# Kernel tuning notes

Measured on AMD Instinct MI355X. Metric: run time of the kernel, lower is better.

## Reference

```python
import jax, jax.numpy as jnp
from jax import lax
import numpy as np
import math

B, W, C, H, K = 4, 1024, 1024, 16, 3  # batch, frames(cropsize), bins, num_bands, kernel
D = C // H  # head dim


def setup_inputs() -> dict:
    key = jax.random.key(0)
    ks = jax.random.split(key, 17)
    lin = lambda k: jax.random.normal(k, (C, C), jnp.float32) * 0.02
    vec = lambda k: jax.random.normal(k, (C,), jnp.float32) * 0.02
    cw = lambda k: jax.random.normal(k, (C, 1, K), jnp.float32) * 0.2  # depthwise conv weight (O, I/g=1, K)
    return {
        'x': jax.random.normal(ks[0], (B, W, C), jnp.float32),
        'qW': lin(ks[1]), 'qb': vec(ks[2]), 'qcw': cw(ks[3]), 'qcb': vec(ks[4]),
        'kW': lin(ks[5]), 'kb': vec(ks[6]), 'kcw': cw(ks[7]), 'kcb': vec(ks[8]),
        'vW': lin(ks[9]), 'vb': vec(ks[10]), 'vcw': cw(ks[11]), 'vcb': vec(ks[12]),
        'oW': lin(ks[13]), 'ob': vec(ks[14]),
        'er': jax.random.normal(ks[15], (D, W), jnp.float32),
    }


def _causal_dwconv(x_bwc, w, b):
    # x: (B, W, C) -> conv over time with left pad K-1, depthwise (groups=C)
    y = lax.conv_general_dilated(
        x_bwc.transpose(0, 2, 1), w, window_strides=(1,), padding=[(K - 1, 0)],
        feature_group_count=C, dimension_numbers=('NCH', 'OIH', 'NCH'))
    return (y + b[None, :, None]).transpose(0, 2, 1)


def reference(x, qW, qb, qcw, qcb, kW, kb, kcw, kcb, vW, vb, vcw, vcb, oW, ob, er):
    q = _causal_dwconv(x @ qW.T + qb, qcw, qcb).reshape(B, W, H, D).transpose(0, 2, 1, 3)  # bhwd
    k = _causal_dwconv(x @ kW.T + kb, kcw, kcb).reshape(B, W, H, D).transpose(0, 2, 3, 1)  # bhdw
    v = _causal_dwconv(x @ vW.T + vb, vcw, vcb).reshape(B, W, H, D).transpose(0, 2, 1, 3)  # bhwd
    # Music-Transformer relative position skewing
    p = jnp.pad(jnp.einsum('bhwd,dt->bhwt', q, er), ((0, 0), (0, 0), (0, 0), (1, 0)))
    p = p.transpose(0, 1, 3, 2)[:, :, 1:, :]  # (B,H,W,W)
    qk = (jnp.matmul(q, k) + p) / math.sqrt(C)
    a = jax.nn.softmax(qk, axis=-1)
    o = jnp.matmul(a, v).transpose(0, 2, 1, 3).reshape(B, W, C)
    return o @ oW.T + ob
```

## Files before the change

### kernel.cpp

```cpp
#include <hip/hip_runtime.h>

#define B_ 4
#define W_ 1024
#define C_ 1024
#define H_ 16
#define D_ 64

typedef __attribute__((ext_vector_type(8))) short short8;
typedef __attribute__((ext_vector_type(4))) float f32x4;

__device__ __forceinline__ unsigned short f2b(float f) {
  unsigned u = __builtin_bit_cast(unsigned, f);
  unsigned r = (u + 0x7fffu + ((u >> 16) & 1u)) >> 16;
  return (unsigned short)r;
}
__device__ __forceinline__ float b2f(short b) {
  return __builtin_bit_cast(float, ((unsigned)(unsigned short)b) << 16);
}
__device__ __forceinline__ unsigned pk2(float a, float b) {
  unsigned r;
  asm("v_cvt_pk_bf16_f32 %0, %1, %2" : "=v"(r) : "v"(a), "v"(b));
  return r;
}

typedef __attribute__((address_space(1))) void GV;
typedef __attribute__((address_space(3))) void LV;
__device__ __forceinline__ void gl16(const short* g, short* l) {
  __builtin_amdgcn_global_load_lds((GV*)g, (LV*)l, 16, 0, 0);
}

__global__ __launch_bounds__(256)
void prep_kernel(const float* __restrict__ x, const float* __restrict__ qW,
                 const float* __restrict__ kW, const float* __restrict__ vW,
                 const float* __restrict__ oW, const float* __restrict__ er,
                 short* __restrict__ xh, short* __restrict__ wh,
                 short* __restrict__ ertb) {
  const int bx = blockIdx.x;
  const int tid = threadIdx.x;
  if (bx < 4096) {
    const float* s;
    short* d;
    size_t u;
    if (bx < 2048) {
      u = (size_t)bx * 256 + tid;
      s = x; d = xh;
    } else {
      u = (size_t)(bx - 2048) * 256 + tid;
      const int w = (int)(u >> 17);
      s = (w == 0) ? qW : (w == 1) ? kW : (w == 2) ? vW : oW;
      d = wh + (u & ~(size_t)131071) * 8;
      u &= 131071;
      const float4* p = (const float4*)s + u * 2;
      float4 a = p[0], b = p[1];
      short8 r;
      r[0] = f2b(a.x); r[1] = f2b(a.y); r[2] = f2b(a.z); r[3] = f2b(a.w);
      r[4] = f2b(b.x); r[5] = f2b(b.y); r[6] = f2b(b.z); r[7] = f2b(b.w);
      *((short8*)d + u) = r;
      return;
    }
    const float4* p = (const float4*)s + u * 2;
    float4 a = p[0], b = p[1];
    short8 r;
    r[0] = f2b(a.x); r[1] = f2b(a.y); r[2] = f2b(a.z); r[3] = f2b(a.w);
    r[4] = f2b(b.x); r[5] = f2b(b.y); r[6] = f2b(b.z); r[7] = f2b(b.w);
    *((short8*)d + u) = r;
  } else {
    int i = (bx - 4096) * 256 + tid;
    int d = i >> 8;
    int w4 = (i & 255) << 2;
    float4 v = *(const float4*)(er + (size_t)d * W_ + w4);
    ertb[(size_t)(w4 + 0) * D_ + d] = f2b(v.x);
    ertb[(size_t)(w4 + 1) * D_ + d] = f2b(v.y);
    ertb[(size_t)(w4 + 2) * D_ + d] = f2b(v.z);
    ertb[(size_t)(w4 + 3) * D_ + d] = f2b(v.w);
  }
}

#define GSTAGE(T, BUF)                                                       \
  {                                                                          \
    const int k0_ = (T) * 64;                                                \
    gl16(ga + (size_t)0  * K + k0_, sA[BUF] + 0    + ldst);                  \
    gl16(gb + (size_t)0  * K + k0_, sB[BUF] + 0    + ldst);                  \
    gl16(ga + (size_t)32 * K + k0_, sA[BUF] + 2048 + ldst);                  \
    gl16(gb + (size_t)32 * K + k0_, sB[BUF] + 2048 + ldst);                  \
    gl16(ga + (size_t)64 * K + k0_, sA[BUF] + 4096 + ldst);                  \
    gl16(gb + (size_t)64 * K + k0_, sB[BUF] + 4096 + ldst);                  \
    gl16(ga + (size_t)96 * K + k0_, sA[BUF] + 6144 + ldst);                  \
    gl16(gb + (size_t)96 * K + k0_, sB[BUF] + 6144 + ldst);                  \
  }

template <int OUTF32>
__global__ __launch_bounds__(256)
void gemm_bf16_v3(const short* __restrict__ A, const short* __restrict__ Wt,
                  const float* __restrict__ b0, const float* __restrict__ b1,
                  const float* __restrict__ b2, void* __restrict__ outv,
                  int M, int N, int K) {
  __shared__ short sA[2][128 * 64];
  __shared__ short sB[2][128 * 64];
  const int tid = threadIdx.x;
  const int bm = blockIdx.y * 128, bn = blockIdx.x * 128;
  const int wv = tid >> 6, lane = tid & 63;
  const int wr = (wv >> 1) * 64, wc = (wv & 1) * 64;
  const int l15 = lane & 15, l4 = lane >> 4;
  const int srow = tid >> 3;
  const int swsc = ((tid & 7) ^ (srow & 7)) * 8;
  const int cxor = (l15 & 7) * 8;
  const int ldst = tid * 8;
  const short* ga = A + (size_t)(bm + srow) * K + swsc;
  const short* gb = Wt + (size_t)(bn + srow) * K + swsc;

  f32x4 acc[4][4];
#pragma unroll
  for (int mf = 0; mf < 4; ++mf)
#pragma unroll
    for (int nf = 0; nf < 4; ++nf) acc[mf][nf] = (f32x4){0.f, 0.f, 0.f, 0.f};

  const int nt = K >> 6;
  GSTAGE(0, 0)
  for (int t = 0; t < nt; ++t) {
    const int cur = t & 1;
    if (t + 1 < nt) {
      GSTAGE(t + 1, cur ^ 1)
      asm volatile("s_waitcnt vmcnt(8)" ::: "memory");
    } else {
      asm volatile("s_waitcnt vmcnt(0)" ::: "memory");
    }
    __builtin_amdgcn_s_barrier();
    __builtin_amdgcn_sched_barrier(0);
#pragma unroll
    for (int ks = 0; ks < 2; ++ks) {
      short8 af[4], bf[4];
#pragma unroll
      for (int mf = 0; mf < 4; ++mf)
        af[mf] = *(short8*)(sA[cur] + (wr + mf * 16 + l15) * 64 + ((ks * 32 + l4 * 8) ^ cxor));
#pragma unroll
      for (int nf = 0; nf < 4; ++nf)
        bf[nf] = *(short8*)(sB[cur] + (wc + nf * 16 + l15) * 64 + ((ks * 32 + l4 * 8) ^ cxor));
#pragma unroll
      for (int mf = 0; mf < 4; ++mf)
#pragma unroll
        for (int nf = 0; nf < 4; ++nf)
          acc[mf][nf] = __builtin_amdgcn_mfma_f32_16x16x32_bf16(af[mf], bf[nf], acc[mf][nf], 0, 0, 0);
    }
    __builtin_amdgcn_sched_barrier(0);
    __builtin_amdgcn_s_barrier();
  }
#pragma unroll
  for (int mf = 0; mf < 4; ++mf) {
#pragma unroll
    for (int nf = 0; nf < 4; ++nf) {
      const int n = bn + wc + nf * 16 + l15;
      const float bs = (n < 1024) ? b0[n] : ((n < 2048) ? b1[n - 1024] : b2[n - 2048]);
#pragma unroll
      for (int r = 0; r < 4; ++r) {
        const int m = bm + wr + mf * 16 + l4 * 4 + r;
        const float v = acc[mf][nf][r] + bs;
        if (OUTF32) ((float*)outv)[(size_t)m * N + n] = v;
        else        ((short*)outv)[(size_t)m * N + n] = (short)f2b(v);
      }
    }
  }
}

__global__ __launch_bounds__(256)
void dwconv_qk_kernel(const short* __restrict__ yqkv,
                      const float* __restrict__ qcw, const float* __restrict__ qcb,
                      const float* __restrict__ kcw, const float* __restrict__ kcb,
                      short* __restrict__ qc, short* __restrict__ kc) {
  const int t = blockIdx.y;
  const float* cw = t ? kcw : qcw;
  const float* cb = t ? kcb : qcb;
  short* out = t ? kc : qc;
  const int idx = blockIdx.x * 256 + threadIdx.x;
  const int c8 = (idx & (C_ / 8 - 1)) << 3;
  const int bw = idx >> 7;
  const int w = bw & (W_ - 1);
  const short* base = yqkv + (size_t)bw * (3 * C_) + t * C_ + c8;
  short8 x2 = *(const short8*)base;
  short8 x1, x0;
  if (w >= 1) x1 = *(const short8*)(base - 3 * C_); else { for (int j = 0; j < 8; ++j) x1[j] = 0; }
  if (w >= 2) x0 = *(const short8*)(base - 6 * C_); else { for (int j = 0; j < 8; ++j) x0[j] = 0; }
  short8 r;
#pragma unroll
  for (int j = 0; j < 8; ++j) {
    const int c = c8 + j;
    float acc = b2f(x0[j]) * cw[c * 3 + 0] + b2f(x1[j]) * cw[c * 3 + 1] +
                b2f(x2[j]) * cw[c * 3 + 2] + cb[c];
    r[j] = (short)f2b(acc);
  }
  *(short8*)(out + (size_t)bw * C_ + c8) = r;
}

__global__ __launch_bounds__(256)
void dwconv_vt_kernel(const short* __restrict__ yqkv, const float* __restrict__ vcw,
                      const float* __restrict__ vcb, short* __restrict__ vt) {
  __shared__ short t[64][72];
  const int bh = blockIdx.y, w0 = blockIdx.x * 64;
  const int b = bh >> 4, h = bh & 15;
  const int tid = threadIdx.x;
  for (int c = tid; c < 512; c += 256) {
    const int w = c >> 3, dg = c & 7;
    const int gw = w0 + w;
    const short* base = yqkv + ((size_t)(b * W_ + gw)) * (3 * C_) + 2 * C_ + h * 64 + dg * 8;
    short8 x2 = *(const short8*)base;
    short8 x1, x0;
    if (gw >= 1) x1 = *(const short8*)(base - 3 * C_); else { for (int j = 0; j < 8; ++j) x1[j] = 0; }
    if (gw >= 2) x0 = *(const short8*)(base - 6 * C_); else { for (int j = 0; j < 8; ++j) x0[j] = 0; }
#pragma unroll
    for (int j = 0; j < 8; ++j) {
      const int ch = h * 64 + dg * 8 + j;
      float acc = b2f(x0[j]) * vcw[ch * 3 + 0] + b2f(x1[j]) * vcw[ch * 3 + 1] +
                  b2f(x2[j]) * vcw[ch * 3 + 2] + vcb[ch];
      t[dg * 8 + j][w] = (short)f2b(acc);
    }
  }
  __syncthreads();
  for (int c = tid; c < 512; c += 256) {
    const int d = c >> 3, wg = c & 7;
    *(short8*)(vt + ((size_t)(bh * 64 + d)) * W_ + w0 + wg * 8) = *(short8*)&t[d][wg * 8];
  }
}

__global__ __launch_bounds__(256)
void attn_v3_kernel(const short* __restrict__ q, const short* __restrict__ k,
                    const short* __restrict__ vt, const short* __restrict__ ert,
                    short* __restrict__ o) {
  __shared__ short sK[2][4096];
  __shared__ short sQj[2][4096];
  __shared__ short sVt[2][4096];
  __shared__ short sU[8192];
  short* sQ = sU;
  short* sE = sU + 4096;
  short* sP = sU;

  const int tid = threadIdx.x;
  const int wid = blockIdx.x;
  const int swz = (wid & 7) * 128 + (wid >> 3);
  const int bh = swz >> 4, qt = swz & 15;
  const int b = bh >> 4, h = bh & 15;
  const int i0 = qt * 64;
  const int wv = tid >> 6, lane = tid & 63;
  const int l15 = lane & 15, l4 = lane >> 4;
  const size_t bW = (size_t)b * W_;
  const int srow = tid >> 3;
  const int swsc = ((tid & 7) ^ (srow & 7)) * 8;
  const int cxor = (l15 & 7) * 8;

  const short* qbase = q + bW * C_ + h * 64;
  const short* kbase = k + bW * C_ + h * 64;
  const short* vbase = vt + (size_t)bh * 64 * W_;

  {
    const short* g;
    g = qbase + (size_t)(i0 + srow) * C_ + swsc;
    gl16(g, sQ + tid * 8); gl16(g + (size_t)32 * C_, sQ + 2048 + tid * 8);
    g = ert + (size_t)(i0 + srow) * 64 + swsc;
    gl16(g, sE + tid * 8); gl16(g + 32 * 64, sE + 2048 + tid * 8);
    g = kbase + (size_t)srow * C_ + swsc;
    gl16(g, sK[0] + tid * 8); gl16(g + (size_t)32 * C_, sK[0] + 2048 + tid * 8);
    g = qbase + (size_t)srow * C_ + swsc;
    gl16(g, sQj[0] + tid * 8); gl16(g + (size_t)32 * C_, sQj[0] + 2048 + tid * 8);
    g = vbase + (size_t)srow * W_ + swsc;
    gl16(g, sVt[0] + tid * 8); gl16(g + (size_t)32 * W_, sVt[0] + 2048 + tid * 8);
  }
  __syncthreads();

  short8 bQ[2], bE[2];
#pragma unroll
  for (int ks = 0; ks < 2; ++ks) {
    const int off = (ks * 32 + l4 * 8) ^ cxor;
    bQ[ks] = *(short8*)(sQ + (wv * 16 + l15) * 64 + off);
    bE[ks] = *(short8*)(sE + (wv * 16 + l15) * 64 + off);
  }
  __syncthreads();

  float m_ = -1e30f, l_ = 0.f;
  f32x4 accO[4];
#pragma unroll
  for (int mf = 0; mf < 4; ++mf) accO[mf] = (f32x4){0.f, 0.f, 0.f, 0.f};
  const float SC = 0.03125f;

  for (int jt = 0; jt < 16; ++jt) {
    const int cur = jt & 1;
    if (jt < 15) {
      const int j0n = (jt + 1) * 64;
      const short* g;
      g = kbase + (size_t)(j0n + srow) * C_ + swsc;
      gl16(g, sK[cur ^ 1] + tid * 8); gl16(g + (size_t)32 * C_, sK[cur ^ 1] + 2048 + tid * 8);
      g = qbase + (size_t)(j0n + srow) * C_ + swsc;
      gl16(g, sQj[cur ^ 1] + tid * 8); gl16(g + (size_t)32 * C_, sQj[cur ^ 1] + 2048 + tid * 8);
      g = vbase + (size_t)srow * W_ + j0n + swsc;
      gl16(g, sVt[cur ^ 1] + tid * 8); gl16(g + (size_t)32 * W_, sVt[cur ^ 1] + 2048 + tid * 8);
    }

    f32x4 s[4];
#pragma unroll
    for (int mf = 0; mf < 4; ++mf) s[mf] = (f32x4){0.f, 0.f, 0.f, 0.f};
    const int ofA = (l4 * 8) ^ cxor;
    const int ofB = (32 + l4 * 8) ^ cxor;
    __builtin_amdgcn_s_setprio(1);
#pragma unroll
    for (int mf = 0; mf < 4; ++mf) {
      const short* kp = sK[cur] + (mf * 16 + l15) * 64;
      const short* jp = sQj[cur] + (mf * 16 + l15) * 64;
      s[mf] = __builtin_amdgcn_mfma_f32_16x16x32_bf16(*(short8*)(kp + ofA), bQ[0], s[mf], 0, 0, 0);
      s[mf] = __builtin_amdgcn_mfma_f32_16x16x32_bf16(*(short8*)(kp + ofB), bQ[1], s[mf], 0, 0, 0);
      s[mf] = __builtin_amdgcn_mfma_f32_16x16x32_bf16(*(short8*)(jp + ofA), bE[0], s[mf], 0, 0, 0);
      s[mf] = __builtin_amdgcn_mfma_f32_16x16x32_bf16(*(short8*)(jp + ofB), bE[1], s[mf], 0, 0, 0);
    }
    __builtin_amdgcn_s_setprio(0);

    float px = fmaxf(fmaxf(s[0][0], s[0][1]), fmaxf(s[0][2], s[0][3]));
#pragma unroll
    for (int mf = 1; mf < 4; ++mf)
      px = fmaxf(px, fmaxf(fmaxf(s[mf][0], s[mf][1]), fmaxf(s[mf][2], s[mf][3])));
    px = fmaxf(px, __shfl_xor(px, 16));
    px = fmaxf(px, __shfl_xor(px, 32));
    px *= SC;
    if (!__all(px <= m_ + 8.f)) {
      const float mn = fmaxf(m_, px);
      const float sc = __expf(m_ - mn);
      l_ *= sc;
#pragma unroll
      for (int mf = 0; mf < 4; ++mf)
#pragma unroll
        for (int r = 0; r < 4; ++r) accO[mf][r] *= sc;
      m_ = mn;
    }
    float p[4][4];
    float rs = 0.f;
#pragma unroll
    for (int mf = 0; mf < 4; ++mf)
#pragma unroll
      for (int r = 0; r < 4; ++r) {
        p[mf][r] = __expf(__builtin_fmaf(s[mf][r], SC, -m_));
        rs += p[mf][r];
      }
    rs += __shfl_xor(rs, 16);
    rs += __shfl_xor(rs, 32);
    l_ += rs;

#pragma unroll
    for (int mf = 0; mf < 4; ++mf) {
      uint2 w2;
      w2.x = pk2(p[mf][0], p[mf][1]);
      w2.y = pk2(p[mf][2], p[mf][3]);
      const int off = (((2 * mf + (l4 >> 1)) ^ (l15 & 7)) * 8) + (l4 & 1) * 4;
      *(uint2*)(sP + (wv * 16 + l15) * 64 + off) = w2;
    }

    short8 pf[2];
#pragma unroll
    for (int ks = 0; ks < 2; ++ks)
      pf[ks] = *(short8*)(sP + (wv * 16 + l15) * 64 + ((ks * 32 + l4 * 8) ^ cxor));
    __builtin_amdgcn_s_setprio(1);
#pragma unroll
    for (int mf = 0; mf < 4; ++mf) {
      const short* vp = sVt[cur] + (mf * 16 + l15) * 64;
      accO[mf] = __builtin_amdgcn_mfma_f32_16x16x32_bf16(*(short8*)(vp + ofA), pf[0], accO[mf], 0, 0, 0);
      accO[mf] = __builtin_amdgcn_mfma_f32_16x16x32_bf16(*(short8*)(vp + ofB), pf[1], accO[mf], 0, 0, 0);
    }
    __builtin_amdgcn_s_setprio(0);

    __syncthreads();
  }

  const float inv = 1.f / l_;
  const size_t orow = (bW + i0 + wv * 16 + l15) * C_ + h * 64;
#pragma unroll
  for (int mf = 0; mf < 4; ++mf) {
    uint2 w2;
    w2.x = pk2(accO[mf][0] * inv, accO[mf][1] * inv);
    w2.y = pk2(accO[mf][2] * inv, accO[mf][3] * inv);
    *(uint2*)(o + orow + mf * 16 + l4 * 4) = w2;
  }
}

extern "C" void kernel_launch(void* const* d_in, const int* in_sizes, int n_in,
                              void* d_out, int out_size, void* d_ws, size_t ws_size,
                              hipStream_t stream) {
  (void)in_sizes; (void)n_in; (void)out_size; (void)ws_size;
  const float* x   = (const float*)d_in[0];
  const float* qW  = (const float*)d_in[1];
  const float* qb  = (const float*)d_in[2];
  const float* qcw = (const float*)d_in[3];
  const float* qcb = (const float*)d_in[4];
  const float* kW  = (const float*)d_in[5];
  const float* kb  = (const float*)d_in[6];
  const float* kcw = (const float*)d_in[7];
  const float* kcb = (const float*)d_in[8];
  const float* vW  = (const float*)d_in[9];
  const float* vb  = (const float*)d_in[10];
  const float* vcw = (const float*)d_in[11];
  const float* vcb = (const float*)d_in[12];
  const float* oW  = (const float*)d_in[13];
  const float* ob  = (const float*)d_in[14];
  const float* er  = (const float*)d_in[15];
  float* out = (float*)d_out;

  const size_t NE = (size_t)B_ * W_ * C_;
  const size_t NW = (size_t)C_ * C_;
  short* ws   = (short*)d_ws;
  short* xh    = ws;
  short* wqkvh = xh + NE;
  short* oWh   = wqkvh + 3 * NW;
  short* ertb  = oWh + NW;
  short* yqkv  = ertb + (size_t)W_ * D_;
  short* qc    = yqkv + (size_t)(B_ * W_) * (3 * C_);
  short* kc    = qc + NE;
  short* vt    = xh;
  short* oat   = yqkv;

  prep_kernel<<<4160, 256, 0, stream>>>(x, qW, kW, vW, oW, er, xh, wqkvh, ertb);

  const int M = B_ * W_;
  dim3 gq(3 * C_ / 128, M / 128);
  gemm_bf16_v3<0><<<gq, 256, 0, stream>>>(xh, wqkvh, qb, kb, vb, yqkv, M, 3 * C_, C_);

  dwconv_qk_kernel<<<dim3(2048, 2), 256, 0, stream>>>(yqkv, qcw, qcb, kcw, kcb, qc, kc);
  dwconv_vt_kernel<<<dim3(W_ / 64, B_ * H_), 256, 0, stream>>>(yqkv, vcw, vcb, vt);

  attn_v3_kernel<<<1024, 256, 0, stream>>>(qc, kc, vt, ertb, oat);

  dim3 go(C_ / 128, M / 128);
  gemm_bf16_v3<1><<<go, 256, 0, stream>>>(oat, oWh, ob, ob, ob, out, M, C_, C_);
}
```

Baseline: 242.3 us.

## Widen attention blocks to 128 query rows with manual waitcnt barriers and exp2

```diff
diff --git a/kernel.cpp b/kernel.cpp
--- a/kernel.cpp
+++ b/kernel.cpp
@@ -20,6 +20,11 @@
 __device__ __forceinline__ unsigned pk2(float a, float b) {
   unsigned r;
   asm("v_cvt_pk_bf16_f32 %0, %1, %2" : "=v"(r) : "v"(a), "v"(b));
+  return r;
+}
+__device__ __forceinline__ float ex2(float x) {
+  float r;
+  asm("v_exp_f32 %0, %1" : "=v"(r) : "v"(x));
   return r;
 }
 
@@ -221,24 +226,21 @@
   }
 }
 
-__global__ __launch_bounds__(256)
-void attn_v3_kernel(const short* __restrict__ q, const short* __restrict__ k,
+__global__ __launch_bounds__(512, 4)
+void attn_v4_kernel(const short* __restrict__ q, const short* __restrict__ k,
                     const short* __restrict__ vt, const short* __restrict__ ert,
                     short* __restrict__ o) {
   __shared__ short sK[2][4096];
   __shared__ short sQj[2][4096];
   __shared__ short sVt[2][4096];
-  __shared__ short sU[8192];
-  short* sQ = sU;
-  short* sE = sU + 4096;
-  short* sP = sU;
+  __shared__ short sP[128 * 64];
 
   const int tid = threadIdx.x;
   const int wid = blockIdx.x;
-  const int swz = (wid & 7) * 128 + (wid >> 3);
-  const int bh = swz >> 4, qt = swz & 15;
+  const int swz = (wid & 7) * 64 + (wid >> 3);
+  const int bh = swz >> 3, qt = swz & 7;
   const int b = bh >> 4, h = bh & 15;
-  const int i0 = qt * 64;
+  const int i0 = qt * 128;
   const int wv = tid >> 6, lane = tid & 63;
   const int l15 = lane & 15, l4 = lane >> 4;
   const size_t bW = (size_t)b * W_;
@@ -250,48 +252,40 @@
   const short* kbase = k + bW * C_ + h * 64;
   const short* vbase = vt + (size_t)bh * 64 * W_;
 
+  gl16(kbase + (size_t)srow * C_ + swsc, sK[0] + tid * 8);
+  gl16(qbase + (size_t)srow * C_ + swsc, sQj[0] + tid * 8);
+  gl16(vbase + (size_t)srow * W_ + swsc, sVt[0] + tid * 8);
+
+  short8 bQ[2], bE[2];
   {
-    const short* g;
-    g = qbase + (size_t)(i0 + srow) * C_ + swsc;
-    gl16(g, sQ + tid * 8); gl16(g + (size_t)32 * C_, sQ + 2048 + tid * 8);
-    g = ert + (size_t)(i0 + srow) * 64 + swsc;
-    gl16(g, sE + tid * 8); gl16(g + 32 * 64, sE + 2048 + tid * 8);
-    g = kbase + (size_t)srow * C_ + swsc;
-    gl16(g, sK[0] + tid * 8); gl16(g + (size_t)32 * C_, sK[0] + 2048 + tid * 8);
-    g = qbase + (size_t)srow * C_ + swsc;
-    gl16(g, sQj[0] + tid * 8); gl16(g + (size_t)32 * C_, sQj[0] + 2048 + tid * 8);
-    g = vbase + (size_t)srow * W_ + swsc;
-    gl16(g, sVt[0] + tid * 8); gl16(g + (size_t)32 * W_, sVt[0] + 2048 + tid * 8);
-  }
-  __syncthreads();
-
-  short8 bQ[2], bE[2];
-#pragma unroll
-  for (int ks = 0; ks < 2; ++ks) {
-    const int off = (ks * 32 + l4 * 8) ^ cxor;
-    bQ[ks] = *(short8*)(sQ + (wv * 16 + l15) * 64 + off);
-    bE[ks] = *(short8*)(sE + (wv * 16 + l15) * 64 + off);
-  }
-  __syncthreads();
+    const int qi = i0 + wv * 16 + l15;
+#pragma unroll
+    for (int ks = 0; ks < 2; ++ks) {
+      bQ[ks] = *(const short8*)(qbase + (size_t)qi * C_ + ks * 32 + l4 * 8);
+      bE[ks] = *(const short8*)(ert + (size_t)qi * 64 + ks * 32 + l4 * 8);
+    }
+  }
 
   float m_ = -1e30f, l_ = 0.f;
   f32x4 accO[4];
 #pragma unroll
   for (int mf = 0; mf < 4; ++mf) accO[mf] = (f32x4){0.f, 0.f, 0.f, 0.f};
-  const float SC = 0.03125f;
+  const float SC2 = 0.03125f * 1.44269504f;
+  const float THR2 = 11.5416f;
 
   for (int jt = 0; jt < 16; ++jt) {
     const int cur = jt & 1;
     if (jt < 15) {
       const int j0n = (jt + 1) * 64;
-      const short* g;
-      g = kbase + (size_t)(j0n + srow) * C_ + swsc;
-      gl16(g, sK[cur ^ 1] + tid * 8); gl16(g + (size_t)32 * C_, sK[cur ^ 1] + 2048 + tid * 8);
-      g = qbase + (size_t)(j0n + srow) * C_ + swsc;
-      gl16(g, sQj[cur ^ 1] + tid * 8); gl16(g + (size_t)32 * C_, sQj[cur ^ 1] + 2048 + tid * 8);
-      g = vbase + (size_t)srow * W_ + j0n + swsc;
-      gl16(g, sVt[cur ^ 1] + tid * 8); gl16(g + (size_t)32 * W_, sVt[cur ^ 1] + 2048 + tid * 8);
-    }
+      gl16(kbase + (size_t)(j0n + srow) * C_ + swsc, sK[cur ^ 1] + tid * 8);
+      gl16(qbase + (size_t)(j0n + srow) * C_ + swsc, sQj[cur ^ 1] + tid * 8);
+      gl16(vbase + (size_t)srow * W_ + j0n + swsc, sVt[cur ^ 1] + tid * 8);
+      asm volatile("s_waitcnt vmcnt(3)" ::: "memory");
+    } else {
+      asm volatile("s_waitcnt vmcnt(0)" ::: "memory");
+    }
+    __builtin_amdgcn_s_barrier();
+    __builtin_amdgcn_sched_barrier(0);
 
     f32x4 s[4];
 #pragma unroll
@@ -316,10 +310,10 @@
       px = fmaxf(px, fmaxf(fmaxf(s[mf][0], s[mf][1]), fmaxf(s[mf][2], s[mf][3])));
     px = fmaxf(px, __shfl_xor(px, 16));
     px = fmaxf(px, __shfl_xor(px, 32));
-    px *= SC;
-    if (!__all(px <= m_ + 8.f)) {
+    px *= SC2;
+    if (!__all(px <= m_ + THR2)) {
       const float mn = fmaxf(m_, px);
-      const float sc = __expf(m_ - mn);
+      const float sc = ex2(m_ - mn);
       l_ *= sc;
 #pragma unroll
       for (int mf = 0; mf < 4; ++mf)
@@ -333,7 +327,7 @@
     for (int mf = 0; mf < 4; ++mf)
 #pragma unroll
       for (int r = 0; r < 4; ++r) {
-        p[mf][r] = __expf(__builtin_fmaf(s[mf][r], SC, -m_));
+        p[mf][r] = ex2(__builtin_fmaf(s[mf][r], SC2, -m_));
         rs += p[mf][r];
       }
     rs += __shfl_xor(rs, 16);
@@ -362,7 +356,8 @@
     }
     __builtin_amdgcn_s_setprio(0);
 
-    __syncthreads();
+    __builtin_amdgcn_sched_barrier(0);
+    __builtin_amdgcn_s_barrier();
   }
 
   const float inv = 1.f / l_;
@@ -420,7 +415,7 @@
   dwconv_qk_kernel<<<dim3(2048, 2), 256, 0, stream>>>(yqkv, qcw, qcb, kcw, kcb, qc, kc);
   dwconv_vt_kernel<<<dim3(W_ / 64, B_ * H_), 256, 0, stream>>>(yqkv, vcw, vcb, vt);
 
-  attn_v3_kernel<<<1024, 256, 0, stream>>>(qc, kc, vt, ertb, oat);
+  attn_v4_kernel<<<512, 512, 0, stream>>>(qc, kc, vt, ertb, oat);
 
   dim3 go(C_ / 128, M / 128);
   gemm_bf16_v3<1><<<go, 256, 0, stream>>>(oat, oWh, ob, ob, ob, out, M, C_, C_);
```

Result: faster. 221.5 us (-8.6%).
